# Optimization experiments

Measured on AMD Instinct MI355X. Metric: run time of the kernel, lower is better.

The kernel has to match this reference:

```python
import jax, jax.numpy as jnp
import numpy as np

N = 100_000
E = 1_600_000
E_OUT = 400_000
IN_DIM = 16
HID = 128
OUT_DIM = 2
L = 6
BN_EPS = 1e-5


def setup_inputs() -> dict:
    key = jax.random.key(0)
    ks = jax.random.split(key, 8)
    x = jax.random.normal(ks[0], (N, IN_DIM), dtype=jnp.float32)
    edge_index = jax.random.randint(ks[1], (2, E), 0, N, dtype=jnp.int32)
    edge_index_out = jax.random.randint(ks[2], (2, E_OUT), 0, N, dtype=jnp.int32)
    embed_W = jax.random.normal(ks[3], (IN_DIM, HID), jnp.float32) / np.sqrt(IN_DIM)
    embed_b = jnp.zeros((HID,), jnp.float32)
    conv_W = jax.random.normal(ks[4], (L, HID, HID), jnp.float32) / np.sqrt(HID)
    conv_b = jnp.zeros((L, HID), jnp.float32)
    bn_gamma = jnp.ones((L, HID), jnp.float32)
    bn_beta = jnp.zeros((L, HID), jnp.float32)
    layer_weights = jnp.ones((L,), jnp.float32)
    fc_W = jax.random.normal(ks[5], (2 * HID, OUT_DIM), jnp.float32) / np.sqrt(2 * HID)
    fc_b = jnp.zeros((OUT_DIM,), jnp.float32)
    return dict(x=x, edge_index=edge_index, edge_index_out=edge_index_out,
                embed_W=embed_W, embed_b=embed_b, conv_W=conv_W, conv_b=conv_b,
                bn_gamma=bn_gamma, bn_beta=bn_beta, layer_weights=layer_weights,
                fc_W=fc_W, fc_b=fc_b)


def reference(x, edge_index, edge_index_out, embed_W, embed_b, conv_W, conv_b,
              bn_gamma, bn_beta, layer_weights, fc_W, fc_b):
    n = x.shape[0]
    # PyG GCNConv default: add self-loops + symmetric normalization
    loops = jnp.arange(n, dtype=edge_index.dtype)
    src = jnp.concatenate([edge_index[0], loops])
    dst = jnp.concatenate([edge_index[1], loops])
    deg = jax.ops.segment_sum(jnp.ones_like(src, jnp.float32), dst, num_segments=n)
    deg_inv_sqrt = jnp.where(deg > 0, jax.lax.rsqrt(jnp.maximum(deg, 1.0)), 0.0)
    norm = (deg_inv_sqrt[src] * deg_inv_sqrt[dst])[:, None]  # [E+N, 1]

    x_embed = x @ embed_W + embed_b  # [N, HID]
    w = jax.nn.softmax(layer_weights)  # softmax=True path

    for i in range(L):
        h = x_embed @ conv_W[i]                                   # linear
        agg = jax.ops.segment_sum(h[src] * norm, dst, num_segments=n) + conv_b[i]
        # BatchNorm1d, training mode (biased variance)
        mean = jnp.mean(agg, axis=0)
        var = jnp.mean(jnp.square(agg - mean), axis=0)
        hbn = (agg - mean) * jax.lax.rsqrt(var + BN_EPS) * bn_gamma[i] + bn_beta[i]
        x_embed = x_embed + w[i] * jax.nn.relu(hbn)               # weighted residual

    edge_repr = jnp.concatenate([x_embed[edge_index_out[0]], x_embed[edge_index_out[1]]], axis=-1)
    return edge_repr @ fc_W + fc_b
```

## Files before the change

kernel.cpp:

```cpp
#include <hip/hip_runtime.h>


#define NW 8192
#define BKT 128
#define CAP 6144

typedef __attribute__((ext_vector_type(8))) short short8;
typedef __attribute__((ext_vector_type(4))) float f32x4;

static __device__ __forceinline__ unsigned short f2bf(float f) {
  unsigned u = __float_as_uint(f);
  u = u + 0x7fffu + ((u >> 16) & 1u);
  return (unsigned short)(u >> 16);
}
static __device__ __forceinline__ float bf2f_lo(unsigned v) {
  return __uint_as_float(v << 16);
}
static __device__ __forceinline__ float bf2f_hi(unsigned v) {
  return __uint_as_float(v & 0xffff0000u);
}
static __device__ __forceinline__ unsigned pack_bf2(float a, float b) {
  return (unsigned)f2bf(a) | ((unsigned)f2bf(b) << 16);
}
static __device__ __forceinline__ unsigned rfl(unsigned v) {
  return (unsigned)__builtin_amdgcn_readfirstlane((int)v);
}


__global__ __launch_bounds__(256) void hist_bucket_kernel(const int* __restrict__ dst,
                                                          int* __restrict__ bcnt,
                                                          int e, int n, int nbk) {
  __shared__ int h[1024];
  int T = e + n;
  int chunk = (T + gridDim.x - 1) / gridDim.x;
  int j0 = blockIdx.x * chunk;
  int j1 = min(j0 + chunk, T);
  for (int i = threadIdx.x; i < nbk; i += 256) h[i] = 0;
  __syncthreads();
  for (int j = j0 + threadIdx.x; j < j1; j += 256) {
    int d = (j < e) ? dst[j] : (j - e);
    atomicAdd(&h[d >> 7], 1);
  }
  __syncthreads();
  for (int i = threadIdx.x; i < nbk; i += 256)
    if (h[i]) atomicAdd(&bcnt[i], h[i]);
}

__global__ __launch_bounds__(1024) void scan_buckets_kernel(const int* __restrict__ bcnt,
                                                            int* __restrict__ bbase,
                                                            int nbk, int total) {
  __shared__ int lds[1024];
  int t = threadIdx.x;
  int v = (t < nbk) ? bcnt[t] : 0;
  int val = v;
  lds[t] = val; __syncthreads();
  for (int off = 1; off < 1024; off <<= 1) {
    int x = (t >= off) ? lds[t - off] : 0;
    __syncthreads();
    val += x;
    lds[t] = val;
    __syncthreads();
  }
  if (t < nbk) bbase[t] = val - v;
  if (t == 0) bbase[nbk] = total;
}

__global__ __launch_bounds__(256) void scatter_bucket_kernel(const int* __restrict__ src,
                                                             const int* __restrict__ dst,
                                                             int* __restrict__ bfill,
                                                             unsigned* __restrict__ ebuf,
                                                             int e, int n, int nbk) {
  __shared__ int cntL[1024], baseL[1024];
  int T = e + n;
  int chunk = (T + gridDim.x - 1) / gridDim.x;
  int j0 = blockIdx.x * chunk;
  int j1 = min(j0 + chunk, T);
  for (int i = threadIdx.x; i < nbk; i += 256) cntL[i] = 0;
  __syncthreads();
  for (int j = j0 + threadIdx.x; j < j1; j += 256) {
    int d = (j < e) ? dst[j] : (j - e);
    atomicAdd(&cntL[d >> 7], 1);
  }
  __syncthreads();
  for (int i = threadIdx.x; i < nbk; i += 256) {
    int c = cntL[i];
    baseL[i] = c ? atomicAdd(&bfill[i], c) : 0;
    cntL[i] = 0;
  }
  __syncthreads();
  for (int j = j0 + threadIdx.x; j < j1; j += 256) {
    int s, d;
    if (j < e) { s = src[j]; d = dst[j]; } else { s = j - e; d = s; }
    int b = d >> 7;
    int r = atomicAdd(&cntL[b], 1);
    ebuf[baseL[b] + r] = ((unsigned)s << 7) | (unsigned)(d & 127);
  }
}

__global__ __launch_bounds__(256) void sort_bucket_kernel(const int* __restrict__ bbase,
                                                          const unsigned* __restrict__ ebuf,
                                                          int2* __restrict__ ebuf2,
                                                          int* __restrict__ rs,
                                                          float* __restrict__ dis,
                                                          int n, int total) {
  __shared__ unsigned el[CAP];
  __shared__ int hist[BKT], excl[BKT], cur[BKT], scn[BKT];
  int b = blockIdx.x, t = threadIdx.x;
  int e0 = bbase[b], e1 = bbase[b + 1];
  int sz = e1 - e0;
  bool inl = (sz <= CAP);
  if (inl)
    for (int i = t; i < sz; i += 256) el[i] = ebuf[e0 + i];
  if (t < BKT) hist[t] = 0;
  __syncthreads();
  for (int i = t; i < sz; i += 256) {
    unsigned w = inl ? el[i] : ebuf[e0 + i];
    atomicAdd(&hist[w & (BKT - 1)], 1);
  }
  __syncthreads();
  int val = (t < BKT) ? hist[t] : 0;
  if (t < BKT) scn[t] = val;
  __syncthreads();
  for (int off = 1; off < BKT; off <<= 1) {
    int x = (t >= off && t < BKT) ? scn[t - off] : 0;
    __syncthreads();
    if (t < BKT) { val += x; scn[t] = val; }
    __syncthreads();
  }
  if (t < BKT) {
    int ex = val - hist[t];
    excl[t] = ex;
    cur[t] = 0;
    int d = (b << 7) + t;
    if (d < n) {
      rs[d] = e0 + ex;
      dis[d] = rsqrtf((float)hist[t]);
    }
  }
  if (b == 0 && t == 0) rs[n] = total;
  __syncthreads();
  for (int i = t; i < sz; i += 256) {
    unsigned w = inl ? el[i] : ebuf[e0 + i];
    int dl = (int)(w & (BKT - 1));
    int pos = atomicAdd(&cur[dl], 1);
    ebuf2[e0 + excl[dl] + pos] = make_int2((int)(w >> 7), (b << 7) | dl);
  }
}

__global__ void norm_kernel(const int2* __restrict__ ebuf2, const float* __restrict__ dis,
                            int2* __restrict__ esn, int T) {
  int j = blockIdx.x * blockDim.x + threadIdx.x;
  if (j >= T) return;
  int2 p = ebuf2[j];
  float nm = dis[p.x] * dis[p.y];
  unsigned bits = __float_as_uint(nm) & 0xfffffffeu;
  if (j + 1 == T || ebuf2[j + 1].y != p.y) bits |= 1u;
  esn[j] = make_int2(p.x, (int)bits);
}

__global__ void fold_scale_kernel(const int2* __restrict__ esn,
                                  const float* __restrict__ hscale,
                                  unsigned* __restrict__ esnc, int T) {
  int j = blockIdx.x * blockDim.x + threadIdx.x;
  if (j >= T) return;
  int2 p = esn[j];
  unsigned bits = (unsigned)p.y;
  float nm = __uint_as_float(bits & 0xfffffffeu);
  float f = nm * hscale[p.x];
  unsigned fb = __float_as_uint(f) + 0x10000u;
  unsigned field = (fb >> 17) & 0x3fffu;
  esnc[j] = ((unsigned)p.x << 15) | (field << 1) | (bits & 1u);
}

__global__ void wave_bounds_kernel(const int* __restrict__ rs, int* __restrict__ A,
                                   int n, int nw, int eb) {
  int w = blockIdx.x * blockDim.x + threadIdx.x;
  if (w > nw) return;
  int target = w * eb;
  int lo = 0, hi = n;
  while (lo < hi) {
    int mid = (lo + hi) >> 1;
    if (rs[mid] < target) lo = mid + 1; else hi = mid;
  }
  A[w] = lo;
}

__global__ void softmax_w_kernel(const float* __restrict__ lw, float* __restrict__ w, int l) {
  if (threadIdx.x == 0 && blockIdx.x == 0) {
    float m = lw[0];
    for (int i = 1; i < l; ++i) m = fmaxf(m, lw[i]);
    float s = 0.f;
    for (int i = 0; i < l; ++i) s += expf(lw[i] - m);
    for (int i = 0; i < l; ++i) w[i] = expf(lw[i] - m) / s;
  }
}

__global__ void transpose_w_kernel(const float* __restrict__ W, unsigned short* __restrict__ Wt,
                                   int total) {
  int t = blockIdx.x * blockDim.x + threadIdx.x;
  if (t >= total) return;
  int l = t >> 14;
  int nc = (t >> 7) & 127;
  int kk = t & 127;
  Wt[t] = f2bf(W[(size_t)l * 16384 + kk * 128 + nc]);
}


__global__ __launch_bounds__(256) void embed_kernel(const float* __restrict__ x,
                                                    const float* __restrict__ W,
                                                    const float* __restrict__ b,
                                                    unsigned short* __restrict__ xe16, int n) {
  __shared__ float xs[64][20];
  int tid = threadIdx.x;
  int c = tid & 127, half = tid >> 7;
  float wreg[16];
#pragma unroll
  for (int k = 0; k < 16; ++k) wreg[k] = W[k * 128 + c];
  float bc = b[c];
  int ntile = (n + 63) >> 6;
  for (int t = blockIdx.x; t < ntile; t += gridDim.x) {
    int row0 = t * 64;
    {
      int r = tid >> 2, q = tid & 3;
      int row = row0 + r;
      float4 v = (row < n) ? *(const float4*)(x + (size_t)row * 16 + q * 4)
                           : make_float4(0.f, 0.f, 0.f, 0.f);
      *(float4*)&xs[r][q * 4] = v;
    }
    __syncthreads();
    int rbase = half * 32;
    for (int rr = 0; rr < 32; ++rr) {
      int row = row0 + rbase + rr;
      if (row >= n) break;
      float acc = bc;
#pragma unroll
      for (int k = 0; k < 16; ++k) acc = fmaf(xs[rbase + rr][k], wreg[k], acc);
      xe16[(size_t)row * 128 + c] = f2bf(acc);
    }
    __syncthreads();
  }
}


#define EPS 132

template<bool HASBN>
__global__ __launch_bounds__(256) void gemm_fused_kernel(
    const unsigned* __restrict__ aggbf,
    const float* __restrict__ stats8,
    const float* __restrict__ gamma, const float* __restrict__ beta,
    const float* __restrict__ wsm, int layer,
    unsigned* __restrict__ xe16,
    const unsigned short* __restrict__ Wt,
    unsigned char* __restrict__ Hq,
    float* __restrict__ hscale, int n) {
  __shared__ short8 wlds[2048];
  __shared__ unsigned short ep[64 * EPS];
  __shared__ float sc_s[128], sh_s[128];
  int tid = threadIdx.x;
  const short* WtS = (const short*)Wt;
#pragma unroll
  for (int it = 0; it < 8; ++it) {
    int s = it * 256 + tid;
    int ln = s & 63, g = s >> 6;
    int col = ((g >> 2) << 4) + (ln & 15);
    wlds[s] = *(const short8*)(WtS + (size_t)col * 128 + (g & 3) * 32 + (ln >> 4) * 8);
  }
  if (HASBN && tid < 128) {
    float s = 0.f, q = 0.f;
#pragma unroll
    for (int k = 0; k < 8; ++k) {
      s += stats8[k * 256 + tid];
      q += stats8[k * 256 + 128 + tid];
    }
    float invn = 1.f / (float)n;
    float mean = s * invn;
    float var = q * invn - mean * mean;
    float sc = gamma[tid] * rsqrtf(var + 1e-5f);
    sc_s[tid] = sc;
    sh_s[tid] = beta[tid] - mean * sc;
  }
  __syncthreads();

  int wid = tid >> 6, lane = tid & 63;
  int lrow = lane & 15, lk = lane >> 4;
  float wres = HASBN ? wsm[layer] : 0.f;

  int ntiles = (n + 63) >> 6;
  for (int tile = blockIdx.x; tile < ntiles; tile += gridDim.x) {
    int row = tile * 64 + wid * 16 + lrow;
    short8 afrag[4];
    if (row < n) {
      if (HASBN) {
        const unsigned* arow = aggbf + (size_t)row * 64;
        unsigned* xrow = xe16 + (size_t)row * 64;
#pragma unroll
        for (int ks = 0; ks < 4; ++ks) {
          int c0 = ks * 32 + lk * 8;
          uint4 av = *(const uint4*)(arow + (c0 >> 1));
          uint4 xw = *(const uint4*)(xrow + (c0 >> 1));
          unsigned aw[4] = {av.x, av.y, av.z, av.w};
          unsigned xv[4] = {xw.x, xw.y, xw.z, xw.w};
          unsigned xo[4];
          short8 af;
#pragma unroll
          for (int d = 0; d < 4; ++d) {
            int c = c0 + 2 * d;
            float v0 = fmaxf(fmaf(bf2f_lo(aw[d]), sc_s[c], sh_s[c]), 0.f);
            float v1 = fmaxf(fmaf(bf2f_hi(aw[d]), sc_s[c + 1], sh_s[c + 1]), 0.f);
            float xn0 = fmaf(wres, v0, bf2f_lo(xv[d]));
            float xn1 = fmaf(wres, v1, bf2f_hi(xv[d]));
            unsigned pw = pack_bf2(xn0, xn1);
            xo[d] = pw;
            af[2 * d]     = (short)(pw & 0xffff);
            af[2 * d + 1] = (short)(pw >> 16);
          }
          *(uint4*)(xrow + (c0 >> 1)) = make_uint4(xo[0], xo[1], xo[2], xo[3]);
          afrag[ks] = af;
        }
      } else {
        const short* AS = (const short*)xe16;
#pragma unroll
        for (int ks = 0; ks < 4; ++ks)
          afrag[ks] = *(const short8*)(AS + (size_t)row * 128 + ks * 32 + lk * 8);
      }
    } else {
#pragma unroll
      for (int ks = 0; ks < 4; ++ks) afrag[ks] = (short8)0;
    }
    f32x4 acc[8];
#pragma unroll
    for (int n0 = 0; n0 < 8; ++n0) acc[n0] = (f32x4)0.f;
#pragma unroll
    for (int ks = 0; ks < 4; ++ks)
#pragma unroll
      for (int n0 = 0; n0 < 8; ++n0)
        acc[n0] = __builtin_amdgcn_mfma_f32_16x16x32_bf16(
            afrag[ks], wlds[(n0 * 4 + ks) * 64 + lane], acc[n0], 0, 0, 0);

    int eprow0 = wid * 16 + lk * 4;
#pragma unroll
    for (int n0 = 0; n0 < 8; ++n0) {
      int col = n0 * 16 + lrow;
#pragma unroll
      for (int r = 0; r < 4; ++r)
        ep[(eprow0 + r) * EPS + col] = f2bf(acc[n0][r]);
    }
    __syncthreads();
    int trow = tid >> 2;
    int tchunk = tid & 3;
    int orow = tile * 64 + trow;
    const unsigned short* srcl = ep + trow * EPS + tchunk * 32;
    float vals[32];
    float mx = 0.f;
#pragma unroll
    for (int c = 0; c < 4; ++c) {
      short8 ch = *(const short8*)(srcl + c * 8);
#pragma unroll
      for (int i = 0; i < 8; ++i) {
        float v = __uint_as_float(((unsigned)(unsigned short)ch[i]) << 16);
        vals[c * 8 + i] = v;
        mx = fmaxf(mx, __builtin_fabsf(v));
      }
    }
    mx = fmaxf(mx, __shfl_xor(mx, 1));
    mx = fmaxf(mx, __shfl_xor(mx, 2));
    float inv = (mx > 0.f) ? 127.f / mx : 0.f;
    if (orow < n) {
      if (tchunk == 0) hscale[orow] = mx * (1.f / 127.f);
      unsigned q[8];
#pragma unroll
      for (int d = 0; d < 8; ++d) {
        unsigned b = 0;
#pragma unroll
        for (int j = 0; j < 4; ++j) {
          int qi = (int)rintf(vals[d * 4 + j] * inv);
          b |= ((unsigned)(qi & 0xff)) << (8 * j);
        }
        q[d] = b;
      }
      uint4* dst = (uint4*)(Hq + (size_t)orow * 128 + tchunk * 32);
      dst[0] = make_uint4(q[0], q[1], q[2], q[3]);
      dst[1] = make_uint4(q[4], q[5], q[6], q[7]);
    }
    __syncthreads();
  }
}


#define SPMM_STEP(SW, VI)                                                  \
  {                                                                        \
    float fac = __uint_as_float(((SW) & 0x7ffeu) << 16);                   \
    a0 = fmaf(fac, (float)(signed char)((VI) & 0xff), a0);                 \
    a1 = fmaf(fac, (float)(signed char)((VI) >> 8), a1);                   \
    if ((SW) & 1u) {                                                       \
      aggbf[(size_t)row * 64 + lane] = pack_bf2(a0, a1);                   \
      t0 += a0; t1 += a1;                                                  \
      u0 = fmaf(a0, a0, u0); u1 = fmaf(a1, a1, u1);                        \
      a0 = 0.f; a1 = 0.f;                                                  \
      ++row;                                                               \
    }                                                                      \
  }

#define SPMM_GATHER(SW) (*(const unsigned short*)(hqb + (((SW) >> 8) & ~127u) + lane2))

__global__ __launch_bounds__(256) void spmm_kernel(
    const int* __restrict__ rs, const int* __restrict__ A,
    const unsigned* __restrict__ esnc, const unsigned char* __restrict__ hq,
    unsigned* __restrict__ aggbf, float* __restrict__ stats8, int n) {
  int tid = threadIdx.x;
  int wid = tid >> 6, lane = tid & 63;
  int lane2 = lane * 2;
  const char* hqb = (const char*)hq;
  int w = blockIdx.x * 4 + wid;
  int row = __builtin_amdgcn_readfirstlane(A[w]);
  int row_end = __builtin_amdgcn_readfirstlane(A[w + 1]);
  float t0 = 0.f, t1 = 0.f, u0 = 0.f, u1 = 0.f;
  if (row < row_end) {
    int e = __builtin_amdgcn_readfirstlane(rs[row]);
    int eend = __builtin_amdgcn_readfirstlane(rs[row_end]);
    float a0 = 0.f, a1 = 0.f;
    while ((e & 3) && e < eend) {
      unsigned sw = rfl(esnc[e]);
      unsigned v = SPMM_GATHER(sw);
      SPMM_STEP(sw, v)
      ++e;
    }
    const uint4* e4 = (const uint4*)(esnc + e);
    int nq = (eend - e) >> 2;
    int i4 = 0;
    while (i4 + 2 <= nq) {
      uint4 qa = e4[i4], qb = e4[i4 + 1];
      unsigned w0 = rfl(qa.x), w1 = rfl(qa.y), w2 = rfl(qa.z), w3 = rfl(qa.w);
      unsigned w4 = rfl(qb.x), w5 = rfl(qb.y), w6 = rfl(qb.z), w7 = rfl(qb.w);
      unsigned v0 = SPMM_GATHER(w0);
      unsigned v1 = SPMM_GATHER(w1);
      unsigned v2 = SPMM_GATHER(w2);
      unsigned v3 = SPMM_GATHER(w3);
      unsigned v4 = SPMM_GATHER(w4);
      unsigned v5 = SPMM_GATHER(w5);
      unsigned v6 = SPMM_GATHER(w6);
      unsigned v7 = SPMM_GATHER(w7);
      SPMM_STEP(w0, v0) SPMM_STEP(w1, v1)
      SPMM_STEP(w2, v2) SPMM_STEP(w3, v3)
      SPMM_STEP(w4, v4) SPMM_STEP(w5, v5)
      SPMM_STEP(w6, v6) SPMM_STEP(w7, v7)
      i4 += 2;
    }
    e += i4 << 2;
    while (e < eend) {
      unsigned sw = rfl(esnc[e]);
      unsigned v = SPMM_GATHER(sw);
      SPMM_STEP(sw, v)
      ++e;
    }
  }
  __shared__ float red[4][256];
  red[0][tid] = t0; red[1][tid] = t1; red[2][tid] = u0; red[3][tid] = u1;
  __syncthreads();
  float v = red[wid][lane] + red[wid][64 + lane] + red[wid][128 + lane] + red[wid][192 + lane];
  int c = (wid == 0) ? (2 * lane) : (wid == 1) ? (2 * lane + 1)
        : (wid == 2) ? (128 + 2 * lane) : (129 + 2 * lane);
  atomicAdd(&stats8[(blockIdx.x & 7) * 256 + c], v);
}


__global__ __launch_bounds__(256) void fc_node_kernel(
    const unsigned* __restrict__ aggbf, const float* __restrict__ stats8,
    const float* __restrict__ gamma, const float* __restrict__ beta,
    const float* __restrict__ wsm, int layer,
    const unsigned* __restrict__ xe16, const float* __restrict__ fcW,
    float* __restrict__ y, int n) {
  __shared__ float sc_s[128], sh_s[128];
  int tid = threadIdx.x;
  if (tid < 128) {
    float s = 0.f, q = 0.f;
#pragma unroll
    for (int k = 0; k < 8; ++k) {
      s += stats8[k * 256 + tid];
      q += stats8[k * 256 + 128 + tid];
    }
    float invn = 1.f / (float)n;
    float mean = s * invn;
    float var = q * invn - mean * mean;
    float sc = gamma[tid] * rsqrtf(var + 1e-5f);
    sc_s[tid] = sc;
    sh_s[tid] = beta[tid] - mean * sc;
  }
  __syncthreads();
  int wid = tid >> 6, lane = tid & 63;
  int r = blockIdx.x * 4 + wid;
  if (r >= n) return;
  float w = wsm[layer];
  unsigned av = aggbf[(size_t)r * 64 + lane];
  unsigned xv = xe16[(size_t)r * 64 + lane];
  int c0 = lane * 2, c1 = c0 + 1;
  float x0 = fmaf(w, fmaxf(fmaf(bf2f_lo(av), sc_s[c0], sh_s[c0]), 0.f), bf2f_lo(xv));
  float x1 = fmaf(w, fmaxf(fmaf(bf2f_hi(av), sc_s[c1], sh_s[c1]), 0.f), bf2f_hi(xv));
  float a00 = x0 * fcW[c0 * 2 + 0] + x1 * fcW[c1 * 2 + 0];
  float a01 = x0 * fcW[c0 * 2 + 1] + x1 * fcW[c1 * 2 + 1];
  float a10 = x0 * fcW[(128 + c0) * 2 + 0] + x1 * fcW[(128 + c1) * 2 + 0];
  float a11 = x0 * fcW[(128 + c0) * 2 + 1] + x1 * fcW[(128 + c1) * 2 + 1];
#pragma unroll
  for (int off = 32; off; off >>= 1) {
    a00 += __shfl_down(a00, off);
    a01 += __shfl_down(a01, off);
    a10 += __shfl_down(a10, off);
    a11 += __shfl_down(a11, off);
  }
  if (lane == 0) *(float4*)(y + (size_t)r * 4) = make_float4(a00, a01, a10, a11);
}

__global__ void edge_out_kernel(const float* __restrict__ y, const int* __restrict__ eo,
                                const float* __restrict__ fcb, float* __restrict__ out, int m) {
  int j = blockIdx.x * blockDim.x + threadIdx.x;
  if (j >= m) return;
  int a = eo[j], b = eo[m + j];
  float4 ya = *(const float4*)(y + (size_t)a * 4);
  float4 yb = *(const float4*)(y + (size_t)b * 4);
  out[(size_t)j * 2 + 0] = ya.x + yb.z + fcb[0];
  out[(size_t)j * 2 + 1] = ya.y + yb.w + fcb[1];
}


extern "C" void kernel_launch(void* const* d_in, const int* in_sizes, int n_in,
                              void* d_out, int out_size, void* d_ws, size_t ws_size,
                              hipStream_t stream) {
  const float* x     = (const float*)d_in[0];
  const int*   ei    = (const int*)d_in[1];
  const int*   eo    = (const int*)d_in[2];
  const float* embW  = (const float*)d_in[3];
  const float* embB  = (const float*)d_in[4];
  const float* convW = (const float*)d_in[5];
  const float* gamma = (const float*)d_in[7];
  const float* beta  = (const float*)d_in[8];
  const float* lw    = (const float*)d_in[9];
  const float* fcW   = (const float*)d_in[10];
  const float* fcb   = (const float*)d_in[11];
  float* out = (float*)d_out;

  const int n = in_sizes[0] / 16;
  const int e = in_sizes[1] / 2;
  const int m = in_sizes[2] / 2;
  const int L = in_sizes[5] / (128 * 128);

  const int T   = e + n;
  const int EB  = (T + NW - 1) / NW;
  const int nbk = (n + BKT - 1) / BKT;

  const int* esrc = ei;
  const int* edst = ei + e;

  char* wsp = (char*)d_ws;
  size_t off = 0;
  auto take = [&](size_t bytes) -> void* {
    void* p = wsp + off;
    off = (off + bytes + 255) & ~(size_t)255;
    return p;
  };
  int*            bcnt     = (int*)take((size_t)(nbk + 1) * 4);
  int*            bbase    = (int*)take((size_t)(nbk + 1) * 4);
  int*            bfill    = (int*)take((size_t)(nbk + 1) * 4);
  int*            rs       = (int*)take((size_t)(n + 1) * 4);
  float*          dis      = (float*)take((size_t)n * 4);
  float*          hscale   = (float*)take((size_t)n * 4);
  float*          wsm      = (float*)take(64 * 4);
  float*          stats    = (float*)take((size_t)L * 8 * 256 * 4);
  int*            A        = (int*)take((size_t)(NW + 1) * 4);
  unsigned*       ebuf     = (unsigned*)take((size_t)T * 4);
  int2*           ebuf2    = (int2*)take((size_t)T * 8);
  int2*           esn      = (int2*)take((size_t)T * 8);
  unsigned*       esnc     = (unsigned*)take((size_t)T * 4);
  unsigned short* xe16     = (unsigned short*)take((size_t)n * 128 * 2);
  unsigned char*  hq       = (unsigned char*)take((size_t)n * 128);
  unsigned*       aggbf    = (unsigned*)take((size_t)n * 64 * 4);
  unsigned short* Wt       = (unsigned short*)take((size_t)L * 128 * 128 * 2);
  float*          y        = (float*)take((size_t)n * 4 * 4);
  if (off > ws_size || nbk > 1024) return;

  hipMemsetAsync(bcnt, 0, (size_t)(nbk + 1) * 4, stream);
  hipMemsetAsync(stats, 0, (size_t)L * 8 * 256 * 4, stream);
  hist_bucket_kernel<<<512, 256, 0, stream>>>(edst, bcnt, e, n, nbk);
  scan_buckets_kernel<<<1, 1024, 0, stream>>>(bcnt, bbase, nbk, T);
  hipMemcpyAsync(bfill, bbase, (size_t)nbk * 4, hipMemcpyDeviceToDevice, stream);
  scatter_bucket_kernel<<<512, 256, 0, stream>>>(esrc, edst, bfill, ebuf, e, n, nbk);
  sort_bucket_kernel<<<nbk, 256, 0, stream>>>(bbase, ebuf, ebuf2, rs, dis, n, T);
  norm_kernel<<<(T + 255) / 256, 256, 0, stream>>>(ebuf2, dis, esn, T);
  wave_bounds_kernel<<<(NW + 256) / 256, 256, 0, stream>>>(rs, A, n, NW, EB);
  softmax_w_kernel<<<1, 64, 0, stream>>>(lw, wsm, L);
  transpose_w_kernel<<<(L * 16384 + 255) / 256, 256, 0, stream>>>(convW, Wt, L * 16384);

  embed_kernel<<<1024, 256, 0, stream>>>(x, embW, embB, xe16, n);

  const int ntiles = (n + 63) >> 6;
  const int gemm_grid = (ntiles + 1) / 2;
  for (int i = 0; i < L; ++i) {
    if (i == 0) {
      gemm_fused_kernel<false><<<gemm_grid, 256, 0, stream>>>(
          nullptr, nullptr, nullptr, nullptr, wsm, 0, (unsigned*)xe16,
          Wt, hq, hscale, n);
    } else {
      gemm_fused_kernel<true><<<gemm_grid, 256, 0, stream>>>(
          aggbf, stats + (size_t)(i - 1) * 2048,
          gamma + (size_t)(i - 1) * 128, beta + (size_t)(i - 1) * 128, wsm, i - 1,
          (unsigned*)xe16, Wt + (size_t)i * 16384, hq, hscale, n);
    }
    fold_scale_kernel<<<(T + 255) / 256, 256, 0, stream>>>(esn, hscale, esnc, T);
    spmm_kernel<<<NW / 4, 256, 0, stream>>>(rs, A, esnc, hq,
                                            aggbf, stats + (size_t)i * 2048, n);
  }

  fc_node_kernel<<<(n + 3) / 4, 256, 0, stream>>>(
      aggbf, stats + (size_t)(L - 1) * 2048,
      gamma + (size_t)(L - 1) * 128, beta + (size_t)(L - 1) * 128, wsm, L - 1,
      (const unsigned*)xe16, fcW, y, n);
  edge_out_kernel<<<(m + 255) / 256, 256, 0, stream>>>(y, eo, fcb, out, m);
}
```

Baseline: 590.3 us.

## Fuse per-edge scale folding into SpMM via LDS staging; merge setup kernels

Removes the per-layer fold_scale kernel and the esnc intermediate array. Each wave now loads chunks of edge records, folds in the per-source scale and stages the packed records in shared memory before gathering. The three small setup kernels are also merged into one launch. The trade-off is that the SpMM now reads 8-byte records plus a random hscale gather inside its own loop, and adds a chunked staging step with an LDS wait.

```diff
diff --git a/kernel.cpp b/kernel.cpp
--- a/kernel.cpp
+++ b/kernel.cpp
@@ -4,6 +4,7 @@
 #define NW 8192
 #define BKT 128
 #define CAP 6144
+#define CHUNK 512
 
 typedef __attribute__((ext_vector_type(8))) short short8;
 typedef __attribute__((ext_vector_type(4))) float f32x4;
@@ -158,51 +159,36 @@
   esn[j] = make_int2(p.x, (int)bits);
 }
 
-__global__ void fold_scale_kernel(const int2* __restrict__ esn,
-                                  const float* __restrict__ hscale,
-                                  unsigned* __restrict__ esnc, int T) {
-  int j = blockIdx.x * blockDim.x + threadIdx.x;
-  if (j >= T) return;
-  int2 p = esn[j];
-  unsigned bits = (unsigned)p.y;
-  float nm = __uint_as_float(bits & 0xfffffffeu);
-  float f = nm * hscale[p.x];
-  unsigned fb = __float_as_uint(f) + 0x10000u;
-  unsigned field = (fb >> 17) & 0x3fffu;
-  esnc[j] = ((unsigned)p.x << 15) | (field << 1) | (bits & 1u);
-}
-
-__global__ void wave_bounds_kernel(const int* __restrict__ rs, int* __restrict__ A,
-                                   int n, int nw, int eb) {
-  int w = blockIdx.x * blockDim.x + threadIdx.x;
-  if (w > nw) return;
-  int target = w * eb;
-  int lo = 0, hi = n;
-  while (lo < hi) {
-    int mid = (lo + hi) >> 1;
-    if (rs[mid] < target) lo = mid + 1; else hi = mid;
-  }
-  A[w] = lo;
-}
-
-__global__ void softmax_w_kernel(const float* __restrict__ lw, float* __restrict__ w, int l) {
-  if (threadIdx.x == 0 && blockIdx.x == 0) {
+__global__ void misc_kernel(const int* __restrict__ rs, int* __restrict__ A,
+                            int n, int nw, int eb, int wbBlocks,
+                            const float* __restrict__ W, unsigned short* __restrict__ Wt,
+                            int wtotal, int wtBlocks,
+                            const float* __restrict__ lw, float* __restrict__ wsm, int l) {
+  int b = blockIdx.x;
+  if (b < wbBlocks) {
+    int w = b * 256 + threadIdx.x;
+    if (w > nw) return;
+    int target = w * eb;
+    int lo = 0, hi = n;
+    while (lo < hi) {
+      int mid = (lo + hi) >> 1;
+      if (rs[mid] < target) lo = mid + 1; else hi = mid;
+    }
+    A[w] = lo;
+  } else if (b < wbBlocks + wtBlocks) {
+    int t = (b - wbBlocks) * 256 + threadIdx.x;
+    if (t >= wtotal) return;
+    int ll = t >> 14;
+    int nc = (t >> 7) & 127;
+    int kk = t & 127;
+    Wt[t] = f2bf(W[(size_t)ll * 16384 + kk * 128 + nc]);
+  } else if (threadIdx.x == 0) {
     float m = lw[0];
     for (int i = 1; i < l; ++i) m = fmaxf(m, lw[i]);
     float s = 0.f;
     for (int i = 0; i < l; ++i) s += expf(lw[i] - m);
-    for (int i = 0; i < l; ++i) w[i] = expf(lw[i] - m) / s;
-  }
-}
-
-__global__ void transpose_w_kernel(const float* __restrict__ W, unsigned short* __restrict__ Wt,
-                                   int total) {
-  int t = blockIdx.x * blockDim.x + threadIdx.x;
-  if (t >= total) return;
-  int l = t >> 14;
-  int nc = (t >> 7) & 127;
-  int kk = t & 127;
-  Wt[t] = f2bf(W[(size_t)l * 16384 + kk * 128 + nc]);
+    for (int i = 0; i < l; ++i) wsm[i] = expf(lw[i] - m) / s;
+  }
 }
 
 
@@ -406,53 +392,58 @@
 
 __global__ __launch_bounds__(256) void spmm_kernel(
     const int* __restrict__ rs, const int* __restrict__ A,
-    const unsigned* __restrict__ esnc, const unsigned char* __restrict__ hq,
+    const int2* __restrict__ esn, const float* __restrict__ hscale,
+    const unsigned char* __restrict__ hq,
     unsigned* __restrict__ aggbf, float* __restrict__ stats8, int n) {
+  __shared__ unsigned lrec[4][CHUNK];
   int tid = threadIdx.x;
   int wid = tid >> 6, lane = tid & 63;
   int lane2 = lane * 2;
   const char* hqb = (const char*)hq;
+  unsigned* lr = lrec[wid];
   int w = blockIdx.x * 4 + wid;
   int row = __builtin_amdgcn_readfirstlane(A[w]);
   int row_end = __builtin_amdgcn_readfirstlane(A[w + 1]);
   float t0 = 0.f, t1 = 0.f, u0 = 0.f, u1 = 0.f;
   if (row < row_end) {
-    int e = __builtin_amdgcn_readfirstlane(rs[row]);
+    int e0 = __builtin_amdgcn_readfirstlane(rs[row]);
     int eend = __builtin_amdgcn_readfirstlane(rs[row_end]);
     float a0 = 0.f, a1 = 0.f;
-    while ((e & 3) && e < eend) {
-      unsigned sw = rfl(esnc[e]);
-      unsigned v = SPMM_GATHER(sw);
-      SPMM_STEP(sw, v)
-      ++e;
-    }
-    const uint4* e4 = (const uint4*)(esnc + e);
-    int nq = (eend - e) >> 2;
-    int i4 = 0;
-    while (i4 + 2 <= nq) {
-      uint4 qa = e4[i4], qb = e4[i4 + 1];
-      unsigned w0 = rfl(qa.x), w1 = rfl(qa.y), w2 = rfl(qa.z), w3 = rfl(qa.w);
-      unsigned w4 = rfl(qb.x), w5 = rfl(qb.y), w6 = rfl(qb.z), w7 = rfl(qb.w);
-      unsigned v0 = SPMM_GATHER(w0);
-      unsigned v1 = SPMM_GATHER(w1);
-      unsigned v2 = SPMM_GATHER(w2);
-      unsigned v3 = SPMM_GATHER(w3);
-      unsigned v4 = SPMM_GATHER(w4);
-      unsigned v5 = SPMM_GATHER(w5);
-      unsigned v6 = SPMM_GATHER(w6);
-      unsigned v7 = SPMM_GATHER(w7);
-      SPMM_STEP(w0, v0) SPMM_STEP(w1, v1)
-      SPMM_STEP(w2, v2) SPMM_STEP(w3, v3)
-      SPMM_STEP(w4, v4) SPMM_STEP(w5, v5)
-      SPMM_STEP(w6, v6) SPMM_STEP(w7, v7)
-      i4 += 2;
-    }
-    e += i4 << 2;
-    while (e < eend) {
-      unsigned sw = rfl(esnc[e]);
-      unsigned v = SPMM_GATHER(sw);
-      SPMM_STEP(sw, v)
-      ++e;
+    for (int base = e0; base < eend; base += CHUNK) {
+      int cnt = min(CHUNK, eend - base);
+      for (int i = lane; i < cnt; i += 64) {
+        int2 p = esn[base + i];
+        unsigned bits = (unsigned)p.y;
+        float f = __uint_as_float(bits & 0xfffffffeu) * hscale[p.x];
+        unsigned fb = __float_as_uint(f) + 0x10000u;
+        lr[i] = ((unsigned)p.x << 15) | (((fb >> 17) & 0x3fffu) << 1) | (bits & 1u);
+      }
+      __asm__ volatile("s_waitcnt lgkmcnt(0)" ::: "memory");
+      int i = 0;
+      for (; i + 8 <= cnt; i += 8) {
+        uint4 qa = *(const uint4*)(lr + i);
+        uint4 qb = *(const uint4*)(lr + i + 4);
+        unsigned w0 = rfl(qa.x), w1 = rfl(qa.y), w2 = rfl(qa.z), w3 = rfl(qa.w);
+        unsigned w4 = rfl(qb.x), w5 = rfl(qb.y), w6 = rfl(qb.z), w7 = rfl(qb.w);
+        unsigned v0 = SPMM_GATHER(w0);
+        unsigned v1 = SPMM_GATHER(w1);
+        unsigned v2 = SPMM_GATHER(w2);
+        unsigned v3 = SPMM_GATHER(w3);
+        unsigned v4 = SPMM_GATHER(w4);
+        unsigned v5 = SPMM_GATHER(w5);
+        unsigned v6 = SPMM_GATHER(w6);
+        unsigned v7 = SPMM_GATHER(w7);
+        SPMM_STEP(w0, v0) SPMM_STEP(w1, v1)
+        SPMM_STEP(w2, v2) SPMM_STEP(w3, v3)
+        SPMM_STEP(w4, v4) SPMM_STEP(w5, v5)
+        SPMM_STEP(w6, v6) SPMM_STEP(w7, v7)
+      }
+      for (; i < cnt; ++i) {
+        unsigned sw = rfl(lr[i]);
+        unsigned v = SPMM_GATHER(sw);
+        SPMM_STEP(sw, v)
+      }
+      __asm__ volatile("" ::: "memory");
     }
   }
   __shared__ float red[4][256];
@@ -570,7 +561,6 @@
   unsigned*       ebuf     = (unsigned*)take((size_t)T * 4);
   int2*           ebuf2    = (int2*)take((size_t)T * 8);
   int2*           esn      = (int2*)take((size_t)T * 8);
-  unsigned*       esnc     = (unsigned*)take((size_t)T * 4);
   unsigned short* xe16     = (unsigned short*)take((size_t)n * 128 * 2);
   unsigned char*  hq       = (unsigned char*)take((size_t)n * 128);
   unsigned*       aggbf    = (unsigned*)take((size_t)n * 64 * 4);
@@ -586,9 +576,10 @@
   scatter_bucket_kernel<<<512, 256, 0, stream>>>(esrc, edst, bfill, ebuf, e, n, nbk);
   sort_bucket_kernel<<<nbk, 256, 0, stream>>>(bbase, ebuf, ebuf2, rs, dis, n, T);
   norm_kernel<<<(T + 255) / 256, 256, 0, stream>>>(ebuf2, dis, esn, T);
-  wave_bounds_kernel<<<(NW + 256) / 256, 256, 0, stream>>>(rs, A, n, NW, EB);
-  softmax_w_kernel<<<1, 64, 0, stream>>>(lw, wsm, L);
-  transpose_w_kernel<<<(L * 16384 + 255) / 256, 256, 0, stream>>>(convW, Wt, L * 16384);
+  const int wbBlocks = (NW + 256) / 256;
+  const int wtBlocks = (L * 16384 + 255) / 256;
+  misc_kernel<<<wbBlocks + wtBlocks + 1, 256, 0, stream>>>(
+      rs, A, n, NW, EB, wbBlocks, convW, Wt, L * 16384, wtBlocks, lw, wsm, L);
 
   embed_kernel<<<1024, 256, 0, stream>>>(x, embW, embB, xe16, n);
 
@@ -605,8 +596,7 @@
           gamma + (size_t)(i - 1) * 128, beta + (size_t)(i - 1) * 128, wsm, i - 1,
           (unsigned*)xe16, Wt + (size_t)i * 16384, hq, hscale, n);
     }
-    fold_scale_kernel<<<(T + 255) / 256, 256, 0, stream>>>(esn, hscale, esnc, T);
-    spmm_kernel<<<NW / 4, 256, 0, stream>>>(rs, A, esnc, hq,
+    spmm_kernel<<<NW / 4, 256, 0, stream>>>(rs, A, esn, hscale, hq,
                                             aggbf, stats + (size_t)i * 2048, n);
   }
 
```

Result: faster. 560.0 us (-5.1%).
